# Performance work log

Hardware: AMD Instinct MI355X
Metric: run time of the kernel (lower is better)

The kernel has to match this reference:

```python
import jax, jax.numpy as jnp
import numpy as np

KS = 11
SIGMA = 1.5

def _gaussian_kernel(ks=KS, sigma=SIGMA, dtype=jnp.float32):
    ax = jnp.arange(ks, dtype=dtype) - (ks - 1) / 2.0
    xx, yy = jnp.meshgrid(ax, ax, indexing='ij')
    k = jnp.exp(-(xx**2 + yy**2) / (2.0 * sigma * sigma))
    k = k / k.sum()
    return k[None, None, :, :]  # [1,1,ks,ks] (OIHW)

def _conv(x, w):
    pad = KS // 2
    return jax.lax.conv_general_dilated(
        x, w, window_strides=(1, 1), padding=[(pad, pad), (pad, pad)],
        dimension_numbers=('NCHW', 'OIHW', 'NCHW'))

def setup_inputs() -> dict:
    key = jax.random.key(0)
    kx, ky = jax.random.split(key)
    B, H, W = 64, 512, 512
    x = jax.random.uniform(kx, (B, 1, H, W), dtype=jnp.float32)
    y = jax.random.uniform(ky, (B, 1, H, W), dtype=jnp.float32)
    return {"x": x, "y": y}

def reference(x, y):
    w = _gaussian_kernel(dtype=x.dtype)
    mu_x = _conv(x, w)
    mu_y = _conv(y, w)
    mu_x2, mu_y2 = mu_x * mu_x, mu_y * mu_y
    mu_xy = mu_x * mu_y
    sigma_x2 = _conv(x * x, w) - mu_x2
    sigma_y2 = _conv(y * y, w) - mu_y2
    sigma_xy = _conv(x * y, w) - mu_xy
    C1 = 0.01 ** 2
    C2 = 0.03 ** 2
    ssim_map = (2 * mu_xy + C1) * (2 * sigma_xy + C2) / (
        (mu_x2 + mu_y2 + C1) * (sigma_x2 + sigma_y2 + C2) + 1e-12)
    return 1.0 - ssim_map.mean()
```

## Files before the change

kernel.cpp:

```cpp
#include <hip/hip_runtime.h>
#include <math.h>


typedef float v2f __attribute__((ext_vector_type(2)));

#define TS   32
#define HR   42
#define GX   16
#define GY   8
#define NPART (64 * GY * GX)

struct W11 { float w[11]; };

__global__ __launch_bounds__(512) void ssim_main(
    const float* __restrict__ x, const float* __restrict__ y,
    float* __restrict__ partial, W11 wk, int atomic_mode)
{
    __shared__ __align__(16) v2f hst[4][TS * HR];
    __shared__ float red[8];

    const int tid = threadIdx.x;
    const int bx = blockIdx.x, by = blockIdx.y, bz = blockIdx.z;
    const float* __restrict__ xb = x + (size_t)bz * (512 * 512);
    const float* __restrict__ yb = y + (size_t)bz * (512 * 512);
    const int ox = bx * TS;
    const int oy = by * 64;
    const bool colInterior = (bx >= 1) && (bx <= 14);

    if (tid < HR * 8) {
        const int r  = tid >> 3;
        const int c0 = (tid & 7) << 2;
        const int gr = oy - 5 + r;
        const float m0 = ((unsigned)gr        < 512u) ? 1.f : 0.f;
        const float m1 = ((unsigned)(gr + 32) < 512u) ? 1.f : 0.f;
        const v2f  m  = (v2f){m0, m1};
        const int grc0 = min(max(gr, 0), 511);
        const int grc1 = min(max(gr + 32, 0), 511);
        const int gc0 = ox + c0 - 8;

        v2f wxv[14], wyv[14];
        if (colInterior) {
            const float4* px0 = (const float4*)(xb + grc0 * 512 + gc0);
            const float4* px1 = (const float4*)(xb + grc1 * 512 + gc0);
            const float4* py0 = (const float4*)(yb + grc0 * 512 + gc0);
            const float4* py1 = (const float4*)(yb + grc1 * 512 + gc0);
            float4 a[5], b[5], cc[5], d[5];
            #pragma unroll
            for (int kk = 0; kk < 5; ++kk) {
                a[kk]  = px0[kk];
                b[kk]  = px1[kk];
                cc[kk] = py0[kk];
                d[kk]  = py1[kk];
            }
            #pragma unroll
            for (int kk = 0; kk < 5; ++kk) {
                const float ea0[4] = {a[kk].x,  a[kk].y,  a[kk].z,  a[kk].w};
                const float ea1[4] = {b[kk].x,  b[kk].y,  b[kk].z,  b[kk].w};
                const float eb0[4] = {cc[kk].x, cc[kk].y, cc[kk].z, cc[kk].w};
                const float eb1[4] = {d[kk].x,  d[kk].y,  d[kk].z,  d[kk].w};
                #pragma unroll
                for (int e = 0; e < 4; ++e) {
                    const int k = kk * 4 + e;
                    if (k < 3 || k > 16) continue;
                    wxv[k - 3] = (v2f){ea0[e], ea1[e]} * m;
                    wyv[k - 3] = (v2f){eb0[e], eb1[e]} * m;
                }
            }
        } else {
            #pragma unroll
            for (int k = 3; k <= 16; ++k) {
                const int gc  = gc0 + k;
                const int gcc = min(max(gc, 0), 511);
                const float cm = ((unsigned)gc < 512u) ? 1.f : 0.f;
                const v2f mm = m * cm;
                wxv[k - 3] = (v2f){xb[grc0 * 512 + gcc], xb[grc1 * 512 + gcc]} * mm;
                wyv[k - 3] = (v2f){yb[grc0 * 512 + gcc], yb[grc1 * 512 + gcc]} * mm;
            }
        }

        v2f hx[4], hy[4], hss[4], hxy[4];
        #pragma unroll
        for (int o = 0; o < 4; ++o) {
            hx[o] = (v2f)0.f; hy[o] = (v2f)0.f;
            hss[o] = (v2f)0.f; hxy[o] = (v2f)0.f;
        }
        #pragma unroll
        for (int i = 0; i < 14; ++i) {
            const v2f xv = wxv[i], yv = wyv[i];
            const v2f ss = xv * xv + yv * yv;
            const v2f xy = xv * yv;
            #pragma unroll
            for (int o = 0; o < 4; ++o) {
                const int j = i - o;
                if (j < 0 || j > 10) continue;
                const float wj = wk.w[j];
                hx[o]  += wj * xv;
                hy[o]  += wj * yv;
                hss[o] += wj * ss;
                hxy[o] += wj * xy;
            }
        }
        #pragma unroll
        for (int o = 0; o < 4; ++o) {
            const int idx = (c0 + o) * HR + r;
            hst[0][idx] = hx[o];
            hst[1][idx] = hy[o];
            hst[2][idx] = hss[o];
            hst[3][idx] = hxy[o];
        }
    }
    __syncthreads();

    const int c  = tid & 31;
    const int r0 = (tid >> 5) << 1;
    v2f tvq[4][14];
    #pragma unroll
    for (int q = 0; q < 4; ++q) {
        const float4* p4 = (const float4*)&hst[q][c * HR + r0];
        #pragma unroll
        for (int kk = 0; kk < 7; ++kk) {
            const float4 v = p4[kk];
            tvq[q][2 * kk]     = (v2f){v.x, v.y};
            tvq[q][2 * kk + 1] = (v2f){v.z, v.w};
        }
    }
    v2f sq[4][2];
    #pragma unroll
    for (int q = 0; q < 4; ++q) {
        #pragma unroll
        for (int o = 0; o < 2; ++o) {
            v2f a = (v2f)0.f;
            #pragma unroll
            for (int j = 0; j < 11; ++j) a += wk.w[j] * tvq[q][o + j];
            sq[q][o] = a;
        }
    }

    const float C1 = 1e-4f, C2 = 9e-4f;
    float lsum = 0.f;
    #pragma unroll
    for (int o = 0; o < 2; ++o) {
        const v2f mx = sq[0][o], my = sq[1][o];
        const v2f mx2 = mx * mx, my2 = my * my, mxy = mx * my;
        const v2f sig_sum = sq[2][o] - mx2 - my2;
        const v2f sig_xy  = sq[3][o] - mxy;
        const v2f num = (2.f * mxy + C1) * (2.f * sig_xy + C2);
        const v2f den = (mx2 + my2 + C1) * (sig_sum + C2) + 1e-12f;
        lsum += num.x * __builtin_amdgcn_rcpf(den.x)
              + num.y * __builtin_amdgcn_rcpf(den.y);
    }

    #pragma unroll
    for (int off = 32; off; off >>= 1) lsum += __shfl_down(lsum, off);
    if ((tid & 63) == 0) red[tid >> 6] = lsum;
    __syncthreads();
    if (tid == 0) {
        float v = 0.f;
        #pragma unroll
        for (int i = 0; i < 8; ++i) v += red[i];
        if (atomic_mode) atomicAdd(partial, v);
        else partial[(bz * GY + by) * GX + bx] = v;
    }
}

__global__ __launch_bounds__(256) void ssim_fin(const float* __restrict__ partial,
                                                float* __restrict__ out, int n)
{
    float s = 0.f;
    for (int i = threadIdx.x; i < n; i += 256) s += partial[i];
    #pragma unroll
    for (int off = 32; off; off >>= 1) s += __shfl_down(s, off);
    __shared__ float red[4];
    if ((threadIdx.x & 63) == 0) red[threadIdx.x >> 6] = s;
    __syncthreads();
    if (threadIdx.x == 0)
        out[0] = 1.0f - (red[0] + red[1] + red[2] + red[3]) * (1.0f / 16777216.0f);
}

extern "C" void kernel_launch(void* const* d_in, const int* in_sizes, int n_in,
                              void* d_out, int out_size, void* d_ws, size_t ws_size,
                              hipStream_t stream) {
    const float* x = (const float*)d_in[0];
    const float* y = (const float*)d_in[1];
    float* out = (float*)d_out;
    float* ws  = (float*)d_ws;

    W11 wk;
    double e[11], s = 0.0;
    for (int i = 0; i < 11; ++i) {
        double d = (double)i - 5.0;
        e[i] = exp(-(d * d) / 4.5);
        s += e[i];
    }
    for (int i = 0; i < 11; ++i) wk.w[i] = (float)(e[i] / s);

    const bool use_partial = ws_size >= (size_t)NPART * sizeof(float);
    if (!use_partial) hipMemsetAsync(d_ws, 0, sizeof(float), stream);

    hipLaunchKernelGGL(ssim_main, dim3(GX, GY, 64), dim3(512), 0, stream,
                       x, y, ws, wk, use_partial ? 0 : 1);
    hipLaunchKernelGGL(ssim_fin, dim3(1), dim3(256), 0, stream,
                       ws, out, use_partial ? NPART : 1);
}
```

Measured before the change: 252.1 us.

## Pack column pairs instead of row pairs and use a 74-row halo tile

The v2f packing changes from two rows 32 apart to two columns 16 apart. The horizontal pass now covers a 74-row by 32-column tile with one row per thread, loading 36 contiguous floats per thread. This removes the duplicated vertical halo rows of the old row-pair scheme and shrinks the shared-memory staging buffer. In exchange each thread issues wider, partly overlapping global loads and holds more registers, and launch bounds now ask for 4 blocks per CU.

```diff
diff --git a/kernel.cpp b/kernel.cpp
--- a/kernel.cpp
+++ b/kernel.cpp
@@ -4,135 +4,113 @@
 
 typedef float v2f __attribute__((ext_vector_type(2)));
 
-#define TS   32
-#define HR   42
-#define GX   16
-#define GY   8
+#define GX 16
+#define GY 8
 #define NPART (64 * GY * GX)
 
 struct W11 { float w[11]; };
 
-__global__ __launch_bounds__(512) void ssim_main(
+__global__ __launch_bounds__(512, 4) void ssim_main(
     const float* __restrict__ x, const float* __restrict__ y,
     float* __restrict__ partial, W11 wk, int atomic_mode)
 {
-    __shared__ __align__(16) v2f hst[4][TS * HR];
+    __shared__ __align__(16) v2f hst[4][16 * 74];
     __shared__ float red[8];
 
     const int tid = threadIdx.x;
     const int bx = blockIdx.x, by = blockIdx.y, bz = blockIdx.z;
     const float* __restrict__ xb = x + (size_t)bz * (512 * 512);
     const float* __restrict__ yb = y + (size_t)bz * (512 * 512);
-    const int ox = bx * TS;
+    const int ox = bx * 32;
     const int oy = by * 64;
-    const bool colInterior = (bx >= 1) && (bx <= 14);
 
-    if (tid < HR * 8) {
-        const int r  = tid >> 3;
-        const int c0 = (tid & 7) << 2;
+    if (tid < 296) {
+        const int r  = tid >> 2;
+        const int g  = tid & 3;
+        const int c0 = g << 2;
         const int gr = oy - 5 + r;
-        const float m0 = ((unsigned)gr        < 512u) ? 1.f : 0.f;
-        const float m1 = ((unsigned)(gr + 32) < 512u) ? 1.f : 0.f;
-        const v2f  m  = (v2f){m0, m1};
-        const int grc0 = min(max(gr, 0), 511);
-        const int grc1 = min(max(gr + 32, 0), 511);
-        const int gc0 = ox + c0 - 8;
+        const float rm = ((unsigned)gr < 512u) ? 1.f : 0.f;
+        const int grc  = min(max(gr, 0), 511);
+        const int gc0  = ox + c0 - 8;
 
-        v2f wxv[14], wyv[14];
-        if (colInterior) {
-            const float4* px0 = (const float4*)(xb + grc0 * 512 + gc0);
-            const float4* px1 = (const float4*)(xb + grc1 * 512 + gc0);
-            const float4* py0 = (const float4*)(yb + grc0 * 512 + gc0);
-            const float4* py1 = (const float4*)(yb + grc1 * 512 + gc0);
-            float4 a[5], b[5], cc[5], d[5];
+        float fx[36], fy[36];
+        if (bx >= 1 && bx <= 14) {
+            const float4* px = (const float4*)(xb + grc * 512 + gc0);
+            const float4* py = (const float4*)(yb + grc * 512 + gc0);
+            float4 X[9], Y[9];
             #pragma unroll
-            for (int kk = 0; kk < 5; ++kk) {
-                a[kk]  = px0[kk];
-                b[kk]  = px1[kk];
-                cc[kk] = py0[kk];
-                d[kk]  = py1[kk];
-            }
+            for (int k = 0; k < 9; ++k) X[k] = px[k];
             #pragma unroll
-            for (int kk = 0; kk < 5; ++kk) {
-                const float ea0[4] = {a[kk].x,  a[kk].y,  a[kk].z,  a[kk].w};
-                const float ea1[4] = {b[kk].x,  b[kk].y,  b[kk].z,  b[kk].w};
-                const float eb0[4] = {cc[kk].x, cc[kk].y, cc[kk].z, cc[kk].w};
-                const float eb1[4] = {d[kk].x,  d[kk].y,  d[kk].z,  d[kk].w};
-                #pragma unroll
-                for (int e = 0; e < 4; ++e) {
-                    const int k = kk * 4 + e;
-                    if (k < 3 || k > 16) continue;
-                    wxv[k - 3] = (v2f){ea0[e], ea1[e]} * m;
-                    wyv[k - 3] = (v2f){eb0[e], eb1[e]} * m;
-                }
+            for (int k = 0; k < 9; ++k) Y[k] = py[k];
+            #pragma unroll
+            for (int k = 0; k < 9; ++k) {
+                fx[4*k+0] = X[k].x * rm; fx[4*k+1] = X[k].y * rm;
+                fx[4*k+2] = X[k].z * rm; fx[4*k+3] = X[k].w * rm;
+                fy[4*k+0] = Y[k].x * rm; fy[4*k+1] = Y[k].y * rm;
+                fy[4*k+2] = Y[k].z * rm; fy[4*k+3] = Y[k].w * rm;
             }
         } else {
             #pragma unroll
-            for (int k = 3; k <= 16; ++k) {
+            for (int k = 0; k < 36; ++k) {
                 const int gc  = gc0 + k;
                 const int gcc = min(max(gc, 0), 511);
-                const float cm = ((unsigned)gc < 512u) ? 1.f : 0.f;
-                const v2f mm = m * cm;
-                wxv[k - 3] = (v2f){xb[grc0 * 512 + gcc], xb[grc1 * 512 + gcc]} * mm;
-                wyv[k - 3] = (v2f){yb[grc0 * 512 + gcc], yb[grc1 * 512 + gcc]} * mm;
+                const float cm = ((unsigned)gc < 512u) ? rm : 0.f;
+                fx[k] = xb[grc * 512 + gcc] * cm;
+                fy[k] = yb[grc * 512 + gcc] * cm;
             }
         }
 
-        v2f hx[4], hy[4], hss[4], hxy[4];
+        v2f acc[4][4];
         #pragma unroll
-        for (int o = 0; o < 4; ++o) {
-            hx[o] = (v2f)0.f; hy[o] = (v2f)0.f;
-            hss[o] = (v2f)0.f; hxy[o] = (v2f)0.f;
-        }
+        for (int q = 0; q < 4; ++q)
+            #pragma unroll
+            for (int oc = 0; oc < 4; ++oc) acc[q][oc] = (v2f)0.f;
+
         #pragma unroll
-        for (int i = 0; i < 14; ++i) {
-            const v2f xv = wxv[i], yv = wyv[i];
+        for (int k = 0; k < 14; ++k) {
+            const v2f xv = (v2f){fx[3 + k], fx[19 + k]};
+            const v2f yv = (v2f){fy[3 + k], fy[19 + k]};
             const v2f ss = xv * xv + yv * yv;
             const v2f xy = xv * yv;
             #pragma unroll
-            for (int o = 0; o < 4; ++o) {
-                const int j = i - o;
+            for (int oc = 0; oc < 4; ++oc) {
+                const int j = k - oc;
                 if (j < 0 || j > 10) continue;
                 const float wj = wk.w[j];
-                hx[o]  += wj * xv;
-                hy[o]  += wj * yv;
-                hss[o] += wj * ss;
-                hxy[o] += wj * xy;
+                acc[0][oc] += wj * xv;
+                acc[1][oc] += wj * yv;
+                acc[2][oc] += wj * ss;
+                acc[3][oc] += wj * xy;
             }
         }
         #pragma unroll
-        for (int o = 0; o < 4; ++o) {
-            const int idx = (c0 + o) * HR + r;
-            hst[0][idx] = hx[o];
-            hst[1][idx] = hy[o];
-            hst[2][idx] = hss[o];
-            hst[3][idx] = hxy[o];
-        }
+        for (int q = 0; q < 4; ++q)
+            #pragma unroll
+            for (int oc = 0; oc < 4; ++oc)
+                hst[q][(c0 + oc) * 74 + r] = acc[q][oc];
     }
     __syncthreads();
 
-    const int c  = tid & 31;
-    const int r0 = (tid >> 5) << 1;
-    v2f tvq[4][14];
+    const int cp = tid & 15;
+    const int r0 = (tid >> 4) << 1;
+    v2f s[4][2];
     #pragma unroll
     for (int q = 0; q < 4; ++q) {
-        const float4* p4 = (const float4*)&hst[q][c * HR + r0];
+        const float4* p4 = (const float4*)&hst[q][cp * 74 + r0];
+        float4 Q[6];
         #pragma unroll
-        for (int kk = 0; kk < 7; ++kk) {
-            const float4 v = p4[kk];
-            tvq[q][2 * kk]     = (v2f){v.x, v.y};
-            tvq[q][2 * kk + 1] = (v2f){v.z, v.w};
-        }
-    }
-    v2f sq[4][2];
-    #pragma unroll
-    for (int q = 0; q < 4; ++q) {
+        for (int k = 0; k < 6; ++k) Q[k] = p4[k];
         #pragma unroll
         for (int o = 0; o < 2; ++o) {
             v2f a = (v2f)0.f;
             #pragma unroll
-            for (int j = 0; j < 11; ++j) a += wk.w[j] * tvq[q][o + j];
-            sq[q][o] = a;
+            for (int j = 0; j < 11; ++j) {
+                const int t = o + j;
+                const v2f rv = (t & 1) ? (v2f){Q[t >> 1].z, Q[t >> 1].w}
+                                       : (v2f){Q[t >> 1].x, Q[t >> 1].y};
+                a += wk.w[j] * rv;
+            }
+            s[q][o] = a;
         }
     }
 
@@ -140,10 +118,10 @@
     float lsum = 0.f;
     #pragma unroll
     for (int o = 0; o < 2; ++o) {
-        const v2f mx = sq[0][o], my = sq[1][o];
+        const v2f mx = s[0][o], my = s[1][o];
         const v2f mx2 = mx * mx, my2 = my * my, mxy = mx * my;
-        const v2f sig_sum = sq[2][o] - mx2 - my2;
-        const v2f sig_xy  = sq[3][o] - mxy;
+        const v2f sig_sum = s[2][o] - mx2 - my2;
+        const v2f sig_xy  = s[3][o] - mxy;
         const v2f num = (2.f * mxy + C1) * (2.f * sig_xy + C2);
         const v2f den = (mx2 + my2 + C1) * (sig_sum + C2) + 1e-12f;
         lsum += num.x * __builtin_amdgcn_rcpf(den.x)
```

New measurement: 342.9 us. 1.36x slower.
